# Kernel tuning notes

Measured on AMD Instinct MI355X. Metric: run time of the kernel, lower is better.

The kernel has to match this reference:

```python
import jax, jax.numpy as jnp
import numpy as np

SCALE = 0.125  # (dim // heads) ** -0.5 = (256 // 4) ** -0.5


def setup_inputs() -> dict:
    key = jax.random.key(0)
    k1, k2, k3, k4, k5 = jax.random.split(key, 5)
    dim, red = 256, 4
    c = dim // red  # 64
    B, H, W = 4, 64, 64
    x = jax.random.normal(k1, (B, dim, H, W), dtype=jnp.float32)
    qkv_w = jax.random.normal(k2, (3 * c, dim), dtype=jnp.float32) * 0.02
    qkv_b = jax.random.normal(k3, (3 * c,), dtype=jnp.float32) * 0.02
    proj_w = jax.random.normal(k4, (dim, c), dtype=jnp.float32) * 0.02
    proj_b = jax.random.normal(k5, (dim,), dtype=jnp.float32) * 0.02
    return {"x": x, "qkv_w": qkv_w, "qkv_b": qkv_b, "proj_w": proj_w, "proj_b": proj_b}


def reference(x, qkv_w, qkv_b, proj_w, proj_b):
    B, C, H, W = x.shape
    # 1x1 conv == channel matmul
    qkv = jnp.einsum('bchw,oc->bohw', x, qkv_w) + qkv_b[None, :, None, None]
    c = qkv.shape[1] // 3
    qkv = qkv.reshape(B, 3 * c, H * W)
    q, k, v = qkv[:, :c], qkv[:, c:2 * c], qkv[:, 2 * c:]  # [B, c, HW]
    # attn[b, n, m] = sum_c q[b,c,n] * k[b,c,m] * scale
    attn = jnp.einsum('bcn,bcm->bnm', q, k) * SCALE
    attn = jax.nn.softmax(attn, axis=-1)  # [B, HW, HW]
    # out[b, c, n] = sum_m v[b,c,m] * attn[b,n,m]   (v @ attn^T)
    out = jnp.einsum('bcm,bnm->bcn', v, attn).reshape(B, c, H, W)
    # proj 1x1 conv back to dim
    return jnp.einsum('bchw,oc->bohw', out, proj_w) + proj_b[None, :, None, None]
```

## Files before the change

### kernel.cpp

```cpp
#include <hip/hip_runtime.h>
#include <hip/hip_bf16.h>


#define N_TOK 4096
#define CDIM  64
#define DIM   256
#define NBAT  4

typedef __attribute__((ext_vector_type(8)))  short          short8;
typedef __attribute__((ext_vector_type(8)))  unsigned short ushort8_t;
typedef __attribute__((ext_vector_type(4)))  unsigned short ushort4_t;
typedef __attribute__((ext_vector_type(4)))  unsigned int   uint4_t;
typedef __attribute__((ext_vector_type(4)))  float          float4_t;
typedef __attribute__((ext_vector_type(16))) float          float16_t;

#if __has_builtin(__builtin_amdgcn_exp2f)
#define QSC  0.18033688011112042f
#define PEXP(x) __builtin_amdgcn_exp2f(x)
#else
#define QSC  0.125f
#define PEXP(x) __expf(x)
#endif

__device__ __forceinline__ unsigned short f2bf(float f) {
  unsigned int u = __builtin_bit_cast(unsigned int, f);
  u += 0x7fffu + ((u >> 16) & 1u);
  return (unsigned short)(u >> 16);
}

__device__ __forceinline__ unsigned int pkcv(float a, float b) {
  __hip_bfloat162 h = __float22bfloat162_rn(make_float2(a, b));
  unsigned int r; __builtin_memcpy(&r, &h, 4); return r;
}

__device__ __forceinline__ short8 ld8(const unsigned short* p) {
  return __builtin_bit_cast(short8, *(const ushort8_t*)p);
}

__device__ __forceinline__ short8 pack8f(float4_t a, float4_t b) {
  uint4_t u;
  u[0] = pkcv(a[0], a[1]); u[1] = pkcv(a[2], a[3]);
  u[2] = pkcv(b[0], b[1]); u[3] = pkcv(b[2], b[3]);
  return __builtin_bit_cast(short8, u);
}

__device__ __forceinline__ float16_t z16() {
  float16_t r;
#pragma unroll
  for (int i = 0; i < 16; ++i) r[i] = 0.0f;
  return r;
}

typedef __attribute__((address_space(1))) const void* gvp;
typedef __attribute__((address_space(3))) void*       lvp;
__device__ __forceinline__ void dma16(const unsigned short* g, unsigned short* l) {
  __builtin_amdgcn_global_load_lds((gvp)g, (lvp)l, 16, 0, 0);
}

#define MFMA(a, b, c) __builtin_amdgcn_mfma_f32_32x32x16_bf16((a), (b), (c), 0, 0, 0)

#define QOFF  0
#define KOFF  1048576
#define VOFF  2097152
#define WQOFF 3145728
#define BSOFF 3194880

__global__ void k_prep(const float* __restrict__ qw, const float* __restrict__ qb,
                       unsigned short* __restrict__ wqs, float* __restrict__ bs)
{
  const int g = blockIdx.x * 256 + threadIdx.x;
  {
    const int lane = g & 63, grp = g >> 6;
    const int w6 = grp >> 4, kk = grp & 15;
    const int o = w6 * 32 + (lane & 31);
    const int c = kk * 16 + (lane >> 5) * 8;
    const float sc = (o < 64) ? QSC : 1.0f;
    const float* src = qw + o * 256 + c;
    ushort8_t u;
#pragma unroll
    for (int j = 0; j < 8; ++j) u[j] = f2bf(src[j] * sc);
    *(ushort8_t*)(wqs + g * 8) = u;
  }
  if (g < 48) {
    float4_t f = *(const float4_t*)(qb + g * 4);
    float4_t o;
#pragma unroll
    for (int j = 0; j < 4; ++j) o[j] = f[j] * ((g * 4 + j) < 64 ? QSC : 1.0f);
    *(float4_t*)(bs + g * 4) = o;
  }
}

#define RS 132

__global__ __launch_bounds__(768, 3) void k_qkv(
    const float* __restrict__ x, const unsigned short* __restrict__ wqs,
    const float* __restrict__ bs, unsigned short* __restrict__ Qf,
    unsigned short* __restrict__ Kf, unsigned short* __restrict__ Vf)
{
  __shared__ unsigned int Xl[64 * RS];
  const int id = blockIdx.x;
  const int b  = (id >> 1) & 3;
  const int nt = (id & 1) | ((id >> 3) << 1);
  const int t  = threadIdx.x;
  const int n0g = nt * 64;

  if (t < 512) {
    const int n0  = (t & 15) * 4;
    const int cpb = t >> 4;
#pragma unroll
    for (int p = 0; p < 4; ++p) {
      const int cp = cpb + 32 * p, c = cp * 2;
      const float* xb = x + (((size_t)(b * DIM + c)) << 12) + n0g + n0;
      float4_t a = *(const float4_t*)xb;
      float4_t d = *(const float4_t*)(xb + 4096);
#pragma unroll
      for (int j = 0; j < 4; ++j)
        Xl[(n0 + j) * RS + cp] = pkcv(a[j], d[j]);
    }
  }

  const int w = t >> 6, lane = t & 63, l31 = lane & 31, lh = lane >> 5;
  const int ot = w >> 1, sub = w & 1;
  const int ch = nt * 2 + sub;

  const unsigned short* wrow = wqs + ((ot * 16) << 9) + lane * 8;
  short8 wf[16];
#pragma unroll
  for (int kk = 0; kk < 16; ++kk) wf[kk] = ld8(wrow + (kk << 9));

  __syncthreads();

  const unsigned int* xr = &Xl[(sub * 32 + l31) * RS + lh * 4];

  float16_t a0 = z16();
  if (ot < 4) {
#pragma unroll
    for (int kk = 0; kk < 16; ++kk) {
      short8 xf = __builtin_bit_cast(short8, *(const uint4_t*)(xr + kk * 8));
      a0 = MFMA(wf[kk], xf, a0);
    }
  } else {
#pragma unroll
    for (int kk = 0; kk < 16; ++kk) {
      short8 xf = __builtin_bit_cast(short8, *(const uint4_t*)(xr + kk * 8));
      a0 = MFMA(xf, wf[kk], a0);
    }
  }

  if (ot < 4) {
    unsigned short* dst = (ot < 2) ? Qf : Kf;
    const int w2 = ot & 1;
#pragma unroll
    for (int p = 0; p < 4; ++p) {
      const int o = ot * 32 + p * 8 + lh * 4;
      float4_t bv = *(const float4_t*)(bs + o);
      ushort4_t pk4;
#pragma unroll
      for (int q = 0; q < 4; ++q) pk4[q] = f2bf(a0[p * 4 + q] + bv[q]);
      const int kkt = w2 * 2 + (p >> 1);
      *(ushort4_t*)(dst + ((((b * 128 + ch) * 4 + kkt) << 9)
                           + (l31 + 32 * (p & 1)) * 8 + lh * 4)) = pk4;
    }
  } else {
    const int ct = ot - 4;
    const float bvs = bs[128 + ct * 32 + l31];
#pragma unroll
    for (int ks = 0; ks < 2; ++ks) {
      ushort8_t pk8;
#pragma unroll
      for (int j = 0; j < 8; ++j) pk8[j] = f2bf(a0[ks * 8 + j] + bvs);
      *(ushort8_t*)(Vf + ((((b * 128 + ch) * 4 + ct * 2 + ks) << 9)
                          + lane * 8)) = pk8;
    }
  }
}

#define OS   68
#define OLS  72
#define NACC (64 * OS + 64)

__global__ __launch_bounds__(512, 1) void k_attn(
    const unsigned short* __restrict__ Qf, const unsigned short* __restrict__ Kf,
    const unsigned short* __restrict__ Vf, const float* __restrict__ pw,
    const float* __restrict__ pb, float* __restrict__ out)
{
  __shared__ __align__(16) unsigned short Kl[2][32768];
  __shared__ float Oacc[NACC];
  __shared__ __align__(16) unsigned short Ol[64 * OLS];

  const int id = blockIdx.x;
  const int b  = (id >> 1) & 3;
  const int nt = (id & 1) | ((id >> 3) << 1);
  const int t  = threadIdx.x;
  const int wv = t >> 6, lane = t & 63, l31 = lane & 31, lh = lane >> 5;
  const int mq = wv >> 1, nsub = wv & 1;

  for (int i = t; i < NACC; i += 512) Oacc[i] = 0.0f;

  const int wq2 = wv * 2;
  const unsigned short* sg = Kf + (((size_t)(b * 128 + wq2)) << 11) + lane * 8;

  short8 qf[4];
#pragma unroll
  for (int kk = 0; kk < 4; ++kk)
    qf[kk] = ld8(Qf + (((b * 128 + nt * 2 + nsub) * 4 + kk) << 9) + lane * 8);

  const unsigned short* vbase = Vf + (((size_t)(b * 128)) << 11) + lane * 8;

#pragma unroll
  for (int c2 = 0; c2 < 2; ++c2)
#pragma unroll
    for (int kk = 0; kk < 4; ++kk)
      dma16(sg + (c2 << 11) + (kk << 9),
            &Kl[0][((wq2 + c2) << 11) + (kk << 9)]);

  float16_t oc0 = z16(), oc1 = z16();
  float den = 0.0f;

  __syncthreads();

  for (int t8 = 0; t8 < 8; ++t8) {
    const int cur = t8 & 1;

    if (t8 < 7) {
      const unsigned short* g = sg + (((size_t)(t8 + 1)) << 15);
#pragma unroll
      for (int c2 = 0; c2 < 2; ++c2)
#pragma unroll
        for (int kk = 0; kk < 4; ++kk)
          dma16(g + (c2 << 11) + (kk << 9),
                &Kl[cur ^ 1][((wq2 + c2) << 11) + (kk << 9)]);
    }

#pragma unroll
    for (int cc = 0; cc < 4; ++cc) {
      const int ch = mq * 4 + cc;
      const unsigned short* kl = &Kl[cur][ch << 11];

      short8 kf0 = ld8(kl + lane * 8);
      short8 kf1 = ld8(kl + 512 + lane * 8);
      short8 kf2 = ld8(kl + 1024 + lane * 8);
      short8 kf3 = ld8(kl + 1536 + lane * 8);

      float16_t s = z16();
      s = MFMA(kf0, qf[0], s);
      s = MFMA(kf1, qf[1], s);
      s = MFMA(kf2, qf[2], s);
      s = MFMA(kf3, qf[3], s);

      float p[16];
#pragma unroll
      for (int e = 0; e < 16; ++e) p[e] = PEXP(s[e]);
      {
        float d0 = (p[0] + p[1]) + (p[2] + p[3]);
        float d1 = (p[4] + p[5]) + (p[6] + p[7]);
        float d2 = (p[8] + p[9]) + (p[10] + p[11]);
        float d3 = (p[12] + p[13]) + (p[14] + p[15]);
        den += (d0 + d1) + (d2 + d3);
      }

      uint4_t w0, w1;
#pragma unroll
      for (int j = 0; j < 4; ++j) {
        w0[j] = pkcv(p[2 * j], p[2 * j + 1]);
        w1[j] = pkcv(p[8 + 2 * j], p[9 + 2 * j]);
      }
      short8 pf0 = __builtin_bit_cast(short8, w0);
      short8 pf1 = __builtin_bit_cast(short8, w1);

      const unsigned short* vl = vbase + (((size_t)(t8 * 16 + ch)) << 11);
      short8 vf0 = ld8(vl);
      short8 vf1 = ld8(vl + 512);
      short8 vf2 = ld8(vl + 1024);
      short8 vf3 = ld8(vl + 1536);

      oc0 = MFMA(pf0, vf0, oc0);
      oc0 = MFMA(pf1, vf1, oc0);
      oc1 = MFMA(pf0, vf2, oc1);
      oc1 = MFMA(pf1, vf3, oc1);
    }

    __syncthreads();
  }

  den += __shfl_xor(den, 32);

#pragma unroll
  for (int ct = 0; ct < 2; ++ct) {
    const float16_t& oa = ct ? oc1 : oc0;
    const int cc = ct * 32 + l31;
#pragma unroll
    for (int e = 0; e < 16; ++e) {
      const int nr = nsub * 32 + (e & 3) + 8 * (e >> 2) + 4 * lh;
      atomicAdd(&Oacc[nr * OS + cc], oa[e]);
    }
  }
  if (lane < 32) atomicAdd(&Oacc[64 * OS + nsub * 32 + l31], den);
  __syncthreads();

  {
    const int nloc = t >> 3, c8 = (t & 7) * 8;
    float4_t s0 = *(float4_t*)&Oacc[nloc * OS + c8];
    float4_t s1 = *(float4_t*)&Oacc[nloc * OS + c8 + 4];
    const float r = 1.0f / Oacc[64 * OS + nloc];
    uint4_t o4;
    o4[0] = pkcv(s0[0] * r, s0[1] * r);
    o4[1] = pkcv(s0[2] * r, s0[3] * r);
    o4[2] = pkcv(s1[0] * r, s1[1] * r);
    o4[3] = pkcv(s1[2] * r, s1[3] * r);
    *(uint4_t*)&Ol[nloc * OLS + c8] = o4;
  }
  __syncthreads();

  float16_t f0 = z16(), f1 = z16();
  const float* pwrow = pw + (wv * 32 + l31) * 64 + lh * 8;
#pragma unroll
  for (int kk = 0; kk < 4; ++kk) {
    float4_t wa = *(const float4_t*)(pwrow + kk * 16);
    float4_t wb = *(const float4_t*)(pwrow + kk * 16 + 4);
    short8 af = pack8f(wa, wb);
    short8 b0 = ld8(&Ol[l31 * OLS + kk * 16 + lh * 8]);
    short8 b1 = ld8(&Ol[(32 + l31) * OLS + kk * 16 + lh * 8]);
    f0 = MFMA(af, b0, f0);
    f1 = MFMA(af, b1, f1);
  }
  const int n0 = nt * 64;
#pragma unroll
  for (int e = 0; e < 16; ++e) {
    const int o = wv * 32 + (e & 3) + 8 * (e >> 2) + 4 * lh;
    const float bv = pb[o];
    out[((b * 256 + o) << 12) + n0 + l31]      = f0[e] + bv;
    out[((b * 256 + o) << 12) + n0 + 32 + l31] = f1[e] + bv;
  }
}

extern "C" void kernel_launch(void* const* d_in, const int* in_sizes, int n_in,
                              void* d_out, int out_size, void* d_ws, size_t ws_size,
                              hipStream_t stream) {
  const float* x      = (const float*)d_in[0];
  const float* qkv_w  = (const float*)d_in[1];
  const float* qkv_b  = (const float*)d_in[2];
  const float* proj_w = (const float*)d_in[3];
  const float* proj_b = (const float*)d_in[4];
  float* out = (float*)d_out;

  unsigned short* ws  = (unsigned short*)d_ws;
  unsigned short* qf  = ws + QOFF;
  unsigned short* kf  = ws + KOFF;
  unsigned short* vf  = ws + VOFF;
  unsigned short* wqs = ws + WQOFF;
  float*          bs  = (float*)(ws + BSOFF);

  k_prep<<<24, 256, 0, stream>>>(qkv_w, qkv_b, wqs, bs);
  k_qkv<<<256, 768, 0, stream>>>(x, wqs, bs, qf, kf, vf);
  k_attn<<<256, 512, 0, stream>>>(qf, kf, vf, proj_w, proj_b, out);
}
```

Before: 131.0 us.

## Double attention block to 1024 threads and stream K/V directly from global

```diff
diff --git a/kernel.cpp b/kernel.cpp
--- a/kernel.cpp
+++ b/kernel.cpp
@@ -49,12 +49,6 @@
 #pragma unroll
   for (int i = 0; i < 16; ++i) r[i] = 0.0f;
   return r;
-}
-
-typedef __attribute__((address_space(1))) const void* gvp;
-typedef __attribute__((address_space(3))) void*       lvp;
-__device__ __forceinline__ void dma16(const unsigned short* g, unsigned short* l) {
-  __builtin_amdgcn_global_load_lds((gvp)g, (lvp)l, 16, 0, 0);
 }
 
 #define MFMA(a, b, c) __builtin_amdgcn_mfma_f32_32x32x16_bf16((a), (b), (c), 0, 0, 0)
@@ -179,12 +173,11 @@
 #define OLS  72
 #define NACC (64 * OS + 64)
 
-__global__ __launch_bounds__(512, 1) void k_attn(
+__global__ __launch_bounds__(1024) void k_attn(
     const unsigned short* __restrict__ Qf, const unsigned short* __restrict__ Kf,
     const unsigned short* __restrict__ Vf, const float* __restrict__ pw,
     const float* __restrict__ pb, float* __restrict__ out)
 {
-  __shared__ __align__(16) unsigned short Kl[2][32768];
   __shared__ float Oacc[NACC];
   __shared__ __align__(16) unsigned short Ol[64 * OLS];
 
@@ -193,94 +186,60 @@
   const int nt = (id & 1) | ((id >> 3) << 1);
   const int t  = threadIdx.x;
   const int wv = t >> 6, lane = t & 63, l31 = lane & 31, lh = lane >> 5;
-  const int mq = wv >> 1, nsub = wv & 1;
-
-  for (int i = t; i < NACC; i += 512) Oacc[i] = 0.0f;
-
-  const int wq2 = wv * 2;
-  const unsigned short* sg = Kf + (((size_t)(b * 128 + wq2)) << 11) + lane * 8;
+  const int nsub = wv & 1, ms = wv >> 1;
+
+  for (int i = t; i < NACC; i += 1024) Oacc[i] = 0.0f;
 
   short8 qf[4];
 #pragma unroll
   for (int kk = 0; kk < 4; ++kk)
     qf[kk] = ld8(Qf + (((b * 128 + nt * 2 + nsub) * 4 + kk) << 9) + lane * 8);
 
-  const unsigned short* vbase = Vf + (((size_t)(b * 128)) << 11) + lane * 8;
-
-#pragma unroll
-  for (int c2 = 0; c2 < 2; ++c2)
-#pragma unroll
-    for (int kk = 0; kk < 4; ++kk)
-      dma16(sg + (c2 << 11) + (kk << 9),
-            &Kl[0][((wq2 + c2) << 11) + (kk << 9)]);
+  const unsigned short* kb = Kf + (((size_t)(b * 128 + ms)) << 11) + lane * 8;
+  const unsigned short* vb = Vf + (((size_t)(b * 128 + ms)) << 11) + lane * 8;
 
   float16_t oc0 = z16(), oc1 = z16();
   float den = 0.0f;
 
   __syncthreads();
 
-  for (int t8 = 0; t8 < 8; ++t8) {
-    const int cur = t8 & 1;
-
-    if (t8 < 7) {
-      const unsigned short* g = sg + (((size_t)(t8 + 1)) << 15);
-#pragma unroll
-      for (int c2 = 0; c2 < 2; ++c2)
-#pragma unroll
-        for (int kk = 0; kk < 4; ++kk)
-          dma16(g + (c2 << 11) + (kk << 9),
-                &Kl[cur ^ 1][((wq2 + c2) << 11) + (kk << 9)]);
-    }
-
-#pragma unroll
-    for (int cc = 0; cc < 4; ++cc) {
-      const int ch = mq * 4 + cc;
-      const unsigned short* kl = &Kl[cur][ch << 11];
-
-      short8 kf0 = ld8(kl + lane * 8);
-      short8 kf1 = ld8(kl + 512 + lane * 8);
-      short8 kf2 = ld8(kl + 1024 + lane * 8);
-      short8 kf3 = ld8(kl + 1536 + lane * 8);
-
-      float16_t s = z16();
-      s = MFMA(kf0, qf[0], s);
-      s = MFMA(kf1, qf[1], s);
-      s = MFMA(kf2, qf[2], s);
-      s = MFMA(kf3, qf[3], s);
-
-      float p[16];
-#pragma unroll
-      for (int e = 0; e < 16; ++e) p[e] = PEXP(s[e]);
-      {
-        float d0 = (p[0] + p[1]) + (p[2] + p[3]);
-        float d1 = (p[4] + p[5]) + (p[6] + p[7]);
-        float d2 = (p[8] + p[9]) + (p[10] + p[11]);
-        float d3 = (p[12] + p[13]) + (p[14] + p[15]);
-        den += (d0 + d1) + (d2 + d3);
-      }
-
-      uint4_t w0, w1;
-#pragma unroll
-      for (int j = 0; j < 4; ++j) {
-        w0[j] = pkcv(p[2 * j], p[2 * j + 1]);
-        w1[j] = pkcv(p[8 + 2 * j], p[9 + 2 * j]);
-      }
-      short8 pf0 = __builtin_bit_cast(short8, w0);
-      short8 pf1 = __builtin_bit_cast(short8, w1);
-
-      const unsigned short* vl = vbase + (((size_t)(t8 * 16 + ch)) << 11);
-      short8 vf0 = ld8(vl);
-      short8 vf1 = ld8(vl + 512);
-      short8 vf2 = ld8(vl + 1024);
-      short8 vf3 = ld8(vl + 1536);
-
-      oc0 = MFMA(pf0, vf0, oc0);
-      oc0 = MFMA(pf1, vf1, oc0);
-      oc1 = MFMA(pf0, vf2, oc1);
-      oc1 = MFMA(pf1, vf3, oc1);
-    }
-
-    __syncthreads();
+  for (int it = 0; it < 16; ++it) {
+    const size_t o = ((size_t)it) << 14;
+    short8 kf0 = ld8(kb + o),        kf1 = ld8(kb + o + 512);
+    short8 kf2 = ld8(kb + o + 1024), kf3 = ld8(kb + o + 1536);
+    short8 vf0 = ld8(vb + o),        vf1 = ld8(vb + o + 512);
+    short8 vf2 = ld8(vb + o + 1024), vf3 = ld8(vb + o + 1536);
+
+    float16_t s = z16();
+    s = MFMA(kf0, qf[0], s);
+    s = MFMA(kf1, qf[1], s);
+    s = MFMA(kf2, qf[2], s);
+    s = MFMA(kf3, qf[3], s);
+
+    float p[16];
+#pragma unroll
+    for (int e = 0; e < 16; ++e) p[e] = PEXP(s[e]);
+    {
+      float d0 = (p[0] + p[1]) + (p[2] + p[3]);
+      float d1 = (p[4] + p[5]) + (p[6] + p[7]);
+      float d2 = (p[8] + p[9]) + (p[10] + p[11]);
+      float d3 = (p[12] + p[13]) + (p[14] + p[15]);
+      den += (d0 + d1) + (d2 + d3);
+    }
+
+    uint4_t w0, w1;
+#pragma unroll
+    for (int j = 0; j < 4; ++j) {
+      w0[j] = pkcv(p[2 * j], p[2 * j + 1]);
+      w1[j] = pkcv(p[8 + 2 * j], p[9 + 2 * j]);
+    }
+    short8 pf0 = __builtin_bit_cast(short8, w0);
+    short8 pf1 = __builtin_bit_cast(short8, w1);
+
+    oc0 = MFMA(pf0, vf0, oc0);
+    oc0 = MFMA(pf1, vf1, oc0);
+    oc1 = MFMA(pf0, vf2, oc1);
+    oc1 = MFMA(pf1, vf3, oc1);
   }
 
   den += __shfl_xor(den, 32);
@@ -298,7 +257,7 @@
   if (lane < 32) atomicAdd(&Oacc[64 * OS + nsub * 32 + l31], den);
   __syncthreads();
 
-  {
+  if (t < 512) {
     const int nloc = t >> 3, c8 = (t & 7) * 8;
     float4_t s0 = *(float4_t*)&Oacc[nloc * OS + c8];
     float4_t s1 = *(float4_t*)&Oacc[nloc * OS + c8 + 4];
@@ -312,25 +271,24 @@
   }
   __syncthreads();
 
-  float16_t f0 = z16(), f1 = z16();
-  const float* pwrow = pw + (wv * 32 + l31) * 64 + lh * 8;
-#pragma unroll
-  for (int kk = 0; kk < 4; ++kk) {
-    float4_t wa = *(const float4_t*)(pwrow + kk * 16);
-    float4_t wb = *(const float4_t*)(pwrow + kk * 16 + 4);
-    short8 af = pack8f(wa, wb);
-    short8 b0 = ld8(&Ol[l31 * OLS + kk * 16 + lh * 8]);
-    short8 b1 = ld8(&Ol[(32 + l31) * OLS + kk * 16 + lh * 8]);
-    f0 = MFMA(af, b0, f0);
-    f1 = MFMA(af, b1, f1);
-  }
-  const int n0 = nt * 64;
-#pragma unroll
-  for (int e = 0; e < 16; ++e) {
-    const int o = wv * 32 + (e & 3) + 8 * (e >> 2) + 4 * lh;
-    const float bv = pb[o];
-    out[((b * 256 + o) << 12) + n0 + l31]      = f0[e] + bv;
-    out[((b * 256 + o) << 12) + n0 + 32 + l31] = f1[e] + bv;
+  {
+    float16_t f0 = z16();
+    const float* pwrow = pw + (ms * 32 + l31) * 64 + lh * 8;
+#pragma unroll
+    for (int kk = 0; kk < 4; ++kk) {
+      float4_t wa = *(const float4_t*)(pwrow + kk * 16);
+      float4_t wb = *(const float4_t*)(pwrow + kk * 16 + 4);
+      short8 af = pack8f(wa, wb);
+      short8 bfr = ld8(&Ol[(nsub * 32 + l31) * OLS + kk * 16 + lh * 8]);
+      f0 = MFMA(af, bfr, f0);
+    }
+    const int n0 = nt * 64;
+#pragma unroll
+    for (int e = 0; e < 16; ++e) {
+      const int o = ms * 32 + (e & 3) + 8 * (e >> 2) + 4 * lh;
+      const float bv = pb[o];
+      out[((b * 256 + o) << 12) + n0 + nsub * 32 + l31] = f0[e] + bv;
+    }
   }
 }
 
@@ -353,5 +311,5 @@
 
   k_prep<<<24, 256, 0, stream>>>(qkv_w, qkv_b, wqs, bs);
   k_qkv<<<256, 768, 0, stream>>>(x, wqs, bs, qf, kf, vf);
-  k_attn<<<256, 512, 0, stream>>>(qf, kf, vf, proj_w, proj_b, out);
-}
+  k_attn<<<256, 1024, 0, stream>>>(qf, kf, vf, proj_w, proj_b, out);
+}
```

New measurement: 146.2 us. +11.6%, slower.

## Pre-convert x to bf16 MFMA layout in prep kernel, simplify QKV kernel

Applied to the files above, without the earlier changes.

```diff
diff --git a/kernel.cpp b/kernel.cpp
--- a/kernel.cpp
+++ b/kernel.cpp
@@ -64,35 +64,116 @@
 #define VOFF  2097152
 #define WQOFF 3145728
 #define BSOFF 3194880
-
-__global__ void k_prep(const float* __restrict__ qw, const float* __restrict__ qb,
-                       unsigned short* __restrict__ wqs, float* __restrict__ bs)
+#define XFOFF 3276800
+#define WS_NEED_U16 (XFOFF + 4194304)
+
+__global__ void k_prep2(const float* __restrict__ x,
+                        const float* __restrict__ qw, const float* __restrict__ qb,
+                        unsigned short* __restrict__ wqs, float* __restrict__ bs,
+                        unsigned short* __restrict__ xf)
 {
-  const int g = blockIdx.x * 256 + threadIdx.x;
-  {
-    const int lane = g & 63, grp = g >> 6;
-    const int w6 = grp >> 4, kk = grp & 15;
-    const int o = w6 * 32 + (lane & 31);
-    const int c = kk * 16 + (lane >> 5) * 8;
-    const float sc = (o < 64) ? QSC : 1.0f;
-    const float* src = qw + o * 256 + c;
-    ushort8_t u;
-#pragma unroll
-    for (int j = 0; j < 8; ++j) u[j] = f2bf(src[j] * sc);
-    *(ushort8_t*)(wqs + g * 8) = u;
-  }
-  if (g < 48) {
-    float4_t f = *(const float4_t*)(qb + g * 4);
-    float4_t o;
-#pragma unroll
-    for (int j = 0; j < 4; ++j) o[j] = f[j] * ((g * 4 + j) < 64 ? QSC : 1.0f);
-    *(float4_t*)(bs + g * 4) = o;
+  if (blockIdx.x < 24) {
+    const int g = blockIdx.x * 256 + threadIdx.x;
+    {
+      const int lane = g & 63, grp = g >> 6;
+      const int w6 = grp >> 4, kk = grp & 15;
+      const int o = w6 * 32 + (lane & 31);
+      const int c = kk * 16 + (lane >> 5) * 8;
+      const float sc = (o < 64) ? QSC : 1.0f;
+      const float* src = qw + o * 256 + c;
+      ushort8_t u;
+#pragma unroll
+      for (int j = 0; j < 8; ++j) u[j] = f2bf(src[j] * sc);
+      *(ushort8_t*)(wqs + g * 8) = u;
+    }
+    if (g < 48) {
+      float4_t f = *(const float4_t*)(qb + g * 4);
+      float4_t o;
+#pragma unroll
+      for (int j = 0; j < 4; ++j) o[j] = f[j] * ((g * 4 + j) < 64 ? QSC : 1.0f);
+      *(float4_t*)(bs + g * 4) = o;
+    }
+    return;
+  }
+
+  const int idx  = (blockIdx.x - 24) * 256 + threadIdx.x;
+  const int lane = idx & 63;
+  const int kk   = (idx >> 6) & 15;
+  const int ch   = (idx >> 10) & 127;
+  const int b    = (idx >> 17) & 3;
+  const int n    = ch * 32 + (lane & 31);
+  const int c0   = kk * 16 + (lane >> 5) * 8;
+  const float* src = x + (((size_t)(b * DIM + c0)) << 12) + n;
+  ushort8_t u;
+#pragma unroll
+  for (int j = 0; j < 8; ++j) u[j] = f2bf(src[(size_t)j << 12]);
+  *(ushort8_t*)(xf + ((((size_t)(b * 128 + ch)) * 16 + kk) << 9) + lane * 8) = u;
+}
+
+__global__ __launch_bounds__(384, 2) void k_qkv2(
+    const unsigned short* __restrict__ wqs, const float* __restrict__ bs,
+    const unsigned short* __restrict__ xf, unsigned short* __restrict__ Qf,
+    unsigned short* __restrict__ Kf, unsigned short* __restrict__ Vf)
+{
+  const int id = blockIdx.x;
+  const int b  = id >> 7;
+  const int ch = id & 127;
+  const int t  = threadIdx.x;
+  const int ot = t >> 6, lane = t & 63, l31 = lane & 31, lh = lane >> 5;
+
+  const unsigned short* wrow = wqs + ((ot * 16) << 9) + lane * 8;
+  short8 wf[16];
+#pragma unroll
+  for (int kk = 0; kk < 16; ++kk) wf[kk] = ld8(wrow + (kk << 9));
+
+  const unsigned short* xr = xf + (((size_t)(b * 128 + ch)) << 13) + lane * 8;
+
+  float16_t a0 = z16();
+  if (ot < 4) {
+#pragma unroll
+    for (int kk = 0; kk < 16; ++kk) {
+      short8 xv = ld8(xr + (kk << 9));
+      a0 = MFMA(wf[kk], xv, a0);
+    }
+  } else {
+#pragma unroll
+    for (int kk = 0; kk < 16; ++kk) {
+      short8 xv = ld8(xr + (kk << 9));
+      a0 = MFMA(xv, wf[kk], a0);
+    }
+  }
+
+  if (ot < 4) {
+    unsigned short* dst = (ot < 2) ? Qf : Kf;
+    const int w2 = ot & 1;
+#pragma unroll
+    for (int p = 0; p < 4; ++p) {
+      const int o = ot * 32 + p * 8 + lh * 4;
+      float4_t bv = *(const float4_t*)(bs + o);
+      ushort4_t pk4;
+#pragma unroll
+      for (int q = 0; q < 4; ++q) pk4[q] = f2bf(a0[p * 4 + q] + bv[q]);
+      const int kkt = w2 * 2 + (p >> 1);
+      *(ushort4_t*)(dst + ((((b * 128 + ch) * 4 + kkt) << 9)
+                           + (l31 + 32 * (p & 1)) * 8 + lh * 4)) = pk4;
+    }
+  } else {
+    const int ct = ot - 4;
+    const float bvs = bs[128 + ct * 32 + l31];
+#pragma unroll
+    for (int ks = 0; ks < 2; ++ks) {
+      ushort8_t pk8;
+#pragma unroll
+      for (int j = 0; j < 8; ++j) pk8[j] = f2bf(a0[ks * 8 + j] + bvs);
+      *(ushort8_t*)(Vf + ((((b * 128 + ch) * 4 + ct * 2 + ks) << 9)
+                          + lane * 8)) = pk8;
+    }
   }
 }
 
 #define RS 132
 
-__global__ __launch_bounds__(768, 3) void k_qkv(
+__global__ __launch_bounds__(768, 3) void k_qkv_fb(
     const float* __restrict__ x, const unsigned short* __restrict__ wqs,
     const float* __restrict__ bs, unsigned short* __restrict__ Qf,
     unsigned short* __restrict__ Kf, unsigned short* __restrict__ Vf)
@@ -136,14 +217,14 @@
   if (ot < 4) {
 #pragma unroll
     for (int kk = 0; kk < 16; ++kk) {
-      short8 xf = __builtin_bit_cast(short8, *(const uint4_t*)(xr + kk * 8));
-      a0 = MFMA(wf[kk], xf, a0);
+      short8 xv = __builtin_bit_cast(short8, *(const uint4_t*)(xr + kk * 8));
+      a0 = MFMA(wf[kk], xv, a0);
     }
   } else {
 #pragma unroll
     for (int kk = 0; kk < 16; ++kk) {
-      short8 xf = __builtin_bit_cast(short8, *(const uint4_t*)(xr + kk * 8));
-      a0 = MFMA(xf, wf[kk], a0);
+      short8 xv = __builtin_bit_cast(short8, *(const uint4_t*)(xr + kk * 8));
+      a0 = MFMA(xv, wf[kk], a0);
     }
   }
 
@@ -350,8 +431,15 @@
   unsigned short* vf  = ws + VOFF;
   unsigned short* wqs = ws + WQOFF;
   float*          bs  = (float*)(ws + BSOFF);
-
-  k_prep<<<24, 256, 0, stream>>>(qkv_w, qkv_b, wqs, bs);
-  k_qkv<<<256, 768, 0, stream>>>(x, wqs, bs, qf, kf, vf);
+  unsigned short* xfr = ws + XFOFF;
+
+  const bool big = ws_size >= (size_t)WS_NEED_U16 * 2;
+  if (big) {
+    k_prep2<<<2072, 256, 0, stream>>>(x, qkv_w, qkv_b, wqs, bs, xfr);
+    k_qkv2<<<512, 384, 0, stream>>>(wqs, bs, xfr, qf, kf, vf);
+  } else {
+    k_prep2<<<24, 256, 0, stream>>>(x, qkv_w, qkv_b, wqs, bs, xfr);
+    k_qkv_fb<<<256, 768, 0, stream>>>(x, wqs, bs, qf, kf, vf);
+  }
   k_attn<<<256, 512, 0, stream>>>(qf, kf, vf, proj_w, proj_b, out);
 }
```

After: 133.8 us. +2.2%, slower.

## Fuse weight prep, QKV projection and attention into one persistent kernel

Applied to the files above, without the earlier changes.

```diff
diff --git a/kernel.cpp b/kernel.cpp
--- a/kernel.cpp
+++ b/kernel.cpp
@@ -59,130 +59,35 @@
 
 #define MFMA(a, b, c) __builtin_amdgcn_mfma_f32_32x32x16_bf16((a), (b), (c), 0, 0, 0)
 
-#define QOFF  0
 #define KOFF  1048576
 #define VOFF  2097152
-#define WQOFF 3145728
-#define BSOFF 3194880
-
-__global__ void k_prep(const float* __restrict__ qw, const float* __restrict__ qb,
-                       unsigned short* __restrict__ wqs, float* __restrict__ bs)
-{
-  const int g = blockIdx.x * 256 + threadIdx.x;
-  {
-    const int lane = g & 63, grp = g >> 6;
-    const int w6 = grp >> 4, kk = grp & 15;
-    const int o = w6 * 32 + (lane & 31);
-    const int c = kk * 16 + (lane >> 5) * 8;
-    const float sc = (o < 64) ? QSC : 1.0f;
-    const float* src = qw + o * 256 + c;
-    ushort8_t u;
-#pragma unroll
-    for (int j = 0; j < 8; ++j) u[j] = f2bf(src[j] * sc);
-    *(ushort8_t*)(wqs + g * 8) = u;
-  }
-  if (g < 48) {
-    float4_t f = *(const float4_t*)(qb + g * 4);
-    float4_t o;
-#pragma unroll
-    for (int j = 0; j < 4; ++j) o[j] = f[j] * ((g * 4 + j) < 64 ? QSC : 1.0f);
-    *(float4_t*)(bs + g * 4) = o;
-  }
-}
-
-#define RS 132
-
-__global__ __launch_bounds__(768, 3) void k_qkv(
-    const float* __restrict__ x, const unsigned short* __restrict__ wqs,
-    const float* __restrict__ bs, unsigned short* __restrict__ Qf,
-    unsigned short* __restrict__ Kf, unsigned short* __restrict__ Vf)
-{
-  __shared__ unsigned int Xl[64 * RS];
-  const int id = blockIdx.x;
-  const int b  = (id >> 1) & 3;
-  const int nt = (id & 1) | ((id >> 3) << 1);
-  const int t  = threadIdx.x;
-  const int n0g = nt * 64;
-
-  if (t < 512) {
-    const int n0  = (t & 15) * 4;
-    const int cpb = t >> 4;
-#pragma unroll
-    for (int p = 0; p < 4; ++p) {
-      const int cp = cpb + 32 * p, c = cp * 2;
-      const float* xb = x + (((size_t)(b * DIM + c)) << 12) + n0g + n0;
-      float4_t a = *(const float4_t*)xb;
-      float4_t d = *(const float4_t*)(xb + 4096);
-#pragma unroll
-      for (int j = 0; j < 4; ++j)
-        Xl[(n0 + j) * RS + cp] = pkcv(a[j], d[j]);
-    }
-  }
-
-  const int w = t >> 6, lane = t & 63, l31 = lane & 31, lh = lane >> 5;
-  const int ot = w >> 1, sub = w & 1;
-  const int ch = nt * 2 + sub;
-
-  const unsigned short* wrow = wqs + ((ot * 16) << 9) + lane * 8;
-  short8 wf[16];
-#pragma unroll
-  for (int kk = 0; kk < 16; ++kk) wf[kk] = ld8(wrow + (kk << 9));
-
-  __syncthreads();
-
-  const unsigned int* xr = &Xl[(sub * 32 + l31) * RS + lh * 4];
-
-  float16_t a0 = z16();
-  if (ot < 4) {
-#pragma unroll
-    for (int kk = 0; kk < 16; ++kk) {
-      short8 xf = __builtin_bit_cast(short8, *(const uint4_t*)(xr + kk * 8));
-      a0 = MFMA(wf[kk], xf, a0);
-    }
-  } else {
-#pragma unroll
-    for (int kk = 0; kk < 16; ++kk) {
-      short8 xf = __builtin_bit_cast(short8, *(const uint4_t*)(xr + kk * 8));
-      a0 = MFMA(xf, wf[kk], a0);
-    }
-  }
-
-  if (ot < 4) {
-    unsigned short* dst = (ot < 2) ? Qf : Kf;
-    const int w2 = ot & 1;
-#pragma unroll
-    for (int p = 0; p < 4; ++p) {
-      const int o = ot * 32 + p * 8 + lh * 4;
-      float4_t bv = *(const float4_t*)(bs + o);
-      ushort4_t pk4;
-#pragma unroll
-      for (int q = 0; q < 4; ++q) pk4[q] = f2bf(a0[p * 4 + q] + bv[q]);
-      const int kkt = w2 * 2 + (p >> 1);
-      *(ushort4_t*)(dst + ((((b * 128 + ch) * 4 + kkt) << 9)
-                           + (l31 + 32 * (p & 1)) * 8 + lh * 4)) = pk4;
-    }
-  } else {
-    const int ct = ot - 4;
-    const float bvs = bs[128 + ct * 32 + l31];
-#pragma unroll
-    for (int ks = 0; ks < 2; ++ks) {
-      ushort8_t pk8;
-#pragma unroll
-      for (int j = 0; j < 8; ++j) pk8[j] = f2bf(a0[ks * 8 + j] + bvs);
-      *(ushort8_t*)(Vf + ((((b * 128 + ch) * 4 + ct * 2 + ks) << 9)
-                          + lane * 8)) = pk8;
-    }
-  }
-}
-
+#define CTOFF 3145728
+
+#define RS   132
 #define OS   68
 #define OLS  72
 #define NACC (64 * OS + 64)
 
-__global__ __launch_bounds__(512, 1) void k_attn(
-    const unsigned short* __restrict__ Qf, const unsigned short* __restrict__ Kf,
-    const unsigned short* __restrict__ Vf, const float* __restrict__ pw,
-    const float* __restrict__ pb, float* __restrict__ out)
+__device__ __forceinline__ void grid_barrier(unsigned int* ctr) {
+  __threadfence();
+  __syncthreads();
+  if (threadIdx.x == 0) {
+    __hip_atomic_fetch_add(ctr, 1u, __ATOMIC_ACQ_REL, __HIP_MEMORY_SCOPE_AGENT);
+    unsigned int v;
+    do {
+      __builtin_amdgcn_s_sleep(2);
+      v = __hip_atomic_load(ctr, __ATOMIC_ACQUIRE, __HIP_MEMORY_SCOPE_AGENT);
+    } while (v < 256u);
+  }
+  __syncthreads();
+}
+
+__global__ __launch_bounds__(512, 1) void k_fused(
+    const float* __restrict__ x, const float* __restrict__ qw,
+    const float* __restrict__ qb, const float* __restrict__ pw,
+    const float* __restrict__ pb, unsigned short* __restrict__ Kf,
+    unsigned short* __restrict__ Vf, float* __restrict__ out,
+    unsigned int* __restrict__ ctr)
 {
   __shared__ __align__(16) unsigned short Kl[2][32768];
   __shared__ float Oacc[NACC];
@@ -193,18 +98,133 @@
   const int nt = (id & 1) | ((id >> 3) << 1);
   const int t  = threadIdx.x;
   const int wv = t >> 6, lane = t & 63, l31 = lane & 31, lh = lane >> 5;
+
+  unsigned short* Ql = &Ol[0];
+
+  {
+    unsigned int* Xl = (unsigned int*)&Kl[0][0];
+    const int n0g = nt * 64;
+
+    {
+      const int n0  = (t & 15) * 4;
+      const int cpb = t >> 4;
+#pragma unroll
+      for (int p = 0; p < 4; ++p) {
+        const int cp = cpb + 32 * p, c = cp * 2;
+        const float* xb = x + (((size_t)(b * DIM + c)) << 12) + n0g + n0;
+        float4_t a = *(const float4_t*)xb;
+        float4_t d = *(const float4_t*)(xb + 4096);
+#pragma unroll
+        for (int j = 0; j < 4; ++j)
+          Xl[(n0 + j) * RS + cp] = pkcv(a[j], d[j]);
+      }
+    }
+
+    short8 wf[16];
+    if (wv < 6) {
+      const float sc = (wv < 2) ? QSC : 1.0f;
+      const float* qwr = qw + (wv * 32 + l31) * 256 + lh * 8;
+#pragma unroll
+      for (int kk = 0; kk < 16; ++kk) {
+        const float* s = qwr + kk * 16;
+        ushort8_t u;
+#pragma unroll
+        for (int j = 0; j < 8; ++j) u[j] = f2bf(s[j] * sc);
+        wf[kk] = __builtin_bit_cast(short8, u);
+      }
+    }
+    __syncthreads();
+
+    if (wv < 6) {
+      const unsigned int* xr0 = &Xl[l31 * RS + lh * 4];
+      const unsigned int* xr1 = &Xl[(32 + l31) * RS + lh * 4];
+      float16_t a0 = z16(), a1 = z16();
+      if (wv < 4) {
+#pragma unroll
+        for (int kk = 0; kk < 16; ++kk) {
+          short8 x0 = __builtin_bit_cast(short8, *(const uint4_t*)(xr0 + kk * 8));
+          short8 x1 = __builtin_bit_cast(short8, *(const uint4_t*)(xr1 + kk * 8));
+          a0 = MFMA(wf[kk], x0, a0);
+          a1 = MFMA(wf[kk], x1, a1);
+        }
+      } else {
+#pragma unroll
+        for (int kk = 0; kk < 16; ++kk) {
+          short8 x0 = __builtin_bit_cast(short8, *(const uint4_t*)(xr0 + kk * 8));
+          short8 x1 = __builtin_bit_cast(short8, *(const uint4_t*)(xr1 + kk * 8));
+          a0 = MFMA(x0, wf[kk], a0);
+          a1 = MFMA(x1, wf[kk], a1);
+        }
+      }
+
+      if (wv < 2) {
+#pragma unroll
+        for (int sub = 0; sub < 2; ++sub) {
+          const float16_t& aa = sub ? a1 : a0;
+#pragma unroll
+          for (int p = 0; p < 4; ++p) {
+            const int o = wv * 32 + p * 8 + lh * 4;
+            float4_t bv = *(const float4_t*)(qb + o);
+            ushort4_t pk4;
+#pragma unroll
+            for (int q = 0; q < 4; ++q)
+              pk4[q] = f2bf(aa[p * 4 + q] + bv[q] * QSC);
+            const int kkt = (wv & 1) * 2 + (p >> 1);
+            *(ushort4_t*)(Ql + (((sub * 4 + kkt) << 9)
+                           + (l31 + 32 * (p & 1)) * 8 + lh * 4)) = pk4;
+          }
+        }
+      } else if (wv < 4) {
+        const int w2 = wv & 1;
+#pragma unroll
+        for (int sub = 0; sub < 2; ++sub) {
+          const float16_t& aa = sub ? a1 : a0;
+          const int ch = nt * 2 + sub;
+#pragma unroll
+          for (int p = 0; p < 4; ++p) {
+            const int o = wv * 32 + p * 8 + lh * 4;
+            float4_t bv = *(const float4_t*)(qb + o);
+            ushort4_t pk4;
+#pragma unroll
+            for (int q = 0; q < 4; ++q) pk4[q] = f2bf(aa[p * 4 + q] + bv[q]);
+            const int kkt = w2 * 2 + (p >> 1);
+            *(ushort4_t*)(Kf + ((((b * 128 + ch) * 4 + kkt) << 9)
+                           + (l31 + 32 * (p & 1)) * 8 + lh * 4)) = pk4;
+          }
+        }
+      } else {
+        const int ct = wv - 4;
+        const float bvs = qb[128 + ct * 32 + l31];
+#pragma unroll
+        for (int sub = 0; sub < 2; ++sub) {
+          const float16_t& aa = sub ? a1 : a0;
+          const int ch = nt * 2 + sub;
+#pragma unroll
+          for (int ks = 0; ks < 2; ++ks) {
+            ushort8_t pk8;
+#pragma unroll
+            for (int j = 0; j < 8; ++j) pk8[j] = f2bf(aa[ks * 8 + j] + bvs);
+            *(ushort8_t*)(Vf + ((((b * 128 + ch) * 4 + ct * 2 + ks) << 9)
+                            + lane * 8)) = pk8;
+          }
+        }
+      }
+    }
+  }
+
+  grid_barrier(ctr);
+
   const int mq = wv >> 1, nsub = wv & 1;
 
   for (int i = t; i < NACC; i += 512) Oacc[i] = 0.0f;
+
+  short8 qf[4];
+#pragma unroll
+  for (int kk = 0; kk < 4; ++kk)
+    qf[kk] = ld8(Ql + ((nsub * 4 + kk) << 9) + lane * 8);
 
   const int wq2 = wv * 2;
   const unsigned short* sg = Kf + (((size_t)(b * 128 + wq2)) << 11) + lane * 8;
-
-  short8 qf[4];
-#pragma unroll
-  for (int kk = 0; kk < 4; ++kk)
-    qf[kk] = ld8(Qf + (((b * 128 + nt * 2 + nsub) * 4 + kk) << 9) + lane * 8);
-
   const unsigned short* vbase = Vf + (((size_t)(b * 128)) << 11) + lane * 8;
 
 #pragma unroll
@@ -345,13 +365,11 @@
   float* out = (float*)d_out;
 
   unsigned short* ws  = (unsigned short*)d_ws;
-  unsigned short* qf  = ws + QOFF;
   unsigned short* kf  = ws + KOFF;
   unsigned short* vf  = ws + VOFF;
-  unsigned short* wqs = ws + WQOFF;
-  float*          bs  = (float*)(ws + BSOFF);
-
-  k_prep<<<24, 256, 0, stream>>>(qkv_w, qkv_b, wqs, bs);
-  k_qkv<<<256, 768, 0, stream>>>(x, wqs, bs, qf, kf, vf);
-  k_attn<<<256, 512, 0, stream>>>(qf, kf, vf, proj_w, proj_b, out);
-}
+  unsigned int*   ctr = (unsigned int*)(ws + CTOFF);
+
+  hipMemsetAsync(ctr, 0, 4, stream);
+  k_fused<<<256, 512, 0, stream>>>(x, qkv_w, qkv_b, proj_w, proj_b,
+                                   kf, vf, out, ctr);
+}
```

After: 190.5 us. +45.4%, slower.
